# Kernel tuning notes

Measured on AMD Instinct MI355X. Metric: run time of the kernel, lower is better.

Reference implementation:

```python
import jax, jax.numpy as jnp
import numpy as np

N_HEAD = 16
NEG = -1e9


def setup_inputs() -> dict:
    key = jax.random.key(0)
    ks = jax.random.split(key, 10)
    b, s, f = 4, 1024, 1024
    h = N_HEAD
    scale = 1.0 / np.sqrt(f).astype(np.float32)
    x = jax.random.normal(ks[0], (b, s, f), jnp.float32)
    str_mat = jax.random.normal(ks[1], (b, h, s, s), jnp.float32)
    # causal binary mask, float as in the torch module (attn_mask == 0.0 test)
    attn_mask = jnp.broadcast_to(jnp.tril(jnp.ones((s, s), jnp.float32))[None, None], (b, 1, s, s))
    Wq = jax.random.normal(ks[2], (f, f), jnp.float32) * scale
    Wk = jax.random.normal(ks[3], (f, f), jnp.float32) * scale
    Wv = jax.random.normal(ks[4], (f, f), jnp.float32) * scale
    Wo = jax.random.normal(ks[5], (f, f), jnp.float32) * scale
    bq = jax.random.normal(ks[6], (f,), jnp.float32) * 0.01
    bk = jax.random.normal(ks[7], (f,), jnp.float32) * 0.01
    bv = jax.random.normal(ks[8], (f,), jnp.float32) * 0.01
    bo = jax.random.normal(ks[9], (f,), jnp.float32) * 0.01
    return {"x": x, "str_mat": str_mat, "attn_mask": attn_mask,
            "Wq": Wq, "bq": bq, "Wk": Wk, "bk": bk,
            "Wv": Wv, "bv": bv, "Wo": Wo, "bo": bo}


def reference(x, str_mat, attn_mask, Wq, bq, Wk, bk, Wv, bv, Wo, bo):
    b, s, f = x.shape
    h = N_HEAD
    d_h = f // h
    # NOTE: original uses .view(b, h, -1, d_h) with NO transpose -> raw reshape
    q = (x @ Wq + bq).reshape(b, h, s, d_h)
    k = (x @ Wk + bk).reshape(b, h, s, d_h)
    v = (x @ Wv + bv).reshape(b, h, s, d_h)
    # structural bias: mask then softmax
    sm = jnp.where(attn_mask == 0.0, NEG, str_mat)
    sm = jax.nn.softmax(sm, axis=-1)
    # scale by d_h (NOT sqrt(d_h)) as in source; second masked_fill in source
    # is non-in-place with result discarded -> no-op, intentionally omitted
    scores = jnp.einsum('bhqd,bhkd->bhqk', q, k) / d_h + sm
    prob = jax.nn.softmax(scores, axis=-1)  # dropout p=0.0
    out = jnp.einsum('bhqk,bhkd->bhqd', prob, v)  # [b,h,s,d_h]
    out = out.transpose(0, 2, 1, 3).reshape(b, s, f)
    return out @ Wo + bo
```

## Files before the change

### kernel.cpp

```cpp
#include <hip/hip_runtime.h>
#include <hip/hip_bf16.h>

#define BB 4
#define SS 1024
#define FF 1024
#define HH 16
#define DH 64

typedef short bf16x8 __attribute__((ext_vector_type(8)));
typedef float f32x4 __attribute__((ext_vector_type(4)));

__device__ __forceinline__ float b2f(unsigned short u) {
    union { unsigned int i; float f; } x; x.i = ((unsigned int)u) << 16; return x.f;
}
__device__ __forceinline__ unsigned short f2b(float f) {
    unsigned int x = __float_as_uint(f);
    unsigned int r = (x + 0x7fffu + ((x >> 16) & 1u)) >> 16;
    return (unsigned short)r;
}
__device__ __forceinline__ int sw(int row, int col) { return col ^ ((row & 7) << 3); }

__device__ __forceinline__ void async_copy16(void* lds, const void* g) {
    __builtin_amdgcn_global_load_lds(
        (const __attribute__((address_space(1))) unsigned int*)g,
        (__attribute__((address_space(3))) unsigned int*)lds, 16, 0, 0);
}

__global__ void cvt_k(const float* __restrict__ in, unsigned short* __restrict__ out, int n) {
    int i = (blockIdx.x * blockDim.x + threadIdx.x) * 4;
    if (i < n) {
        float4 v = *(const float4*)(in + i);
        ushort4 o;
        o.x = f2b(v.x); o.y = f2b(v.y); o.z = f2b(v.z); o.w = f2b(v.w);
        *(ushort4*)(out + i) = o;
    }
}

__global__ void cvtT_k(const float* __restrict__ W0, const float* __restrict__ W1,
                       const float* __restrict__ W2, const float* __restrict__ W3,
                       unsigned short* __restrict__ out) {
    int y = blockIdx.y;
    const float* src = (y == 0) ? W0 : (y == 1) ? W1 : (y == 2) ? W2 : W3;
    unsigned short* dst = out + (size_t)y * FF * FF;
    __shared__ float t[32][33];
    int tile = blockIdx.x;
    int tk = (tile & 31) * 32, tn = (tile >> 5) * 32;
    int r = threadIdx.x >> 3, c4 = (threadIdx.x & 7) * 4;
    float4 v = *(const float4*)&src[(size_t)(tk + r) * FF + tn + c4];
    t[r][c4 + 0] = v.x; t[r][c4 + 1] = v.y; t[r][c4 + 2] = v.z; t[r][c4 + 3] = v.w;
    __syncthreads();
    ushort4 o;
    o.x = f2b(t[c4 + 0][r]); o.y = f2b(t[c4 + 1][r]);
    o.z = f2b(t[c4 + 2][r]); o.w = f2b(t[c4 + 3][r]);
    *(ushort4*)&dst[(size_t)(tn + r) * FF + tk + c4] = o;
}

__global__ void vtrans_k(const unsigned short* __restrict__ V, unsigned short* __restrict__ Vt) {
    int bh = blockIdx.y;
    int sb = blockIdx.x * 64;
    size_t slab = (size_t)bh * SS * DH;
    __shared__ unsigned int tI[64][65];
    int tid = threadIdx.x;
    #pragma unroll
    for (int v = 0; v < 2; v++) {
        int c = tid + v * 256;
        int row = c >> 3, col = (c & 7) * 8;
        uint4 u = *(const uint4*)&V[slab + (size_t)(sb + row) * DH + col];
        const unsigned short* us = (const unsigned short*)&u;
        #pragma unroll
        for (int j = 0; j < 8; j++) tI[row][col + j] = us[j];
    }
    __syncthreads();
    #pragma unroll
    for (int v = 0; v < 2; v++) {
        int c = tid + v * 256;
        int drow = c >> 3, scol = (c & 7) * 8;
        unsigned short o[8];
        #pragma unroll
        for (int j = 0; j < 8; j++) o[j] = (unsigned short)tI[scol + j][drow];
        *(uint4*)&Vt[slab + (size_t)drow * SS + sb + scol] = *(uint4*)o;
    }
}

__global__ __launch_bounds__(256, 3) void gemm32_k(
    const unsigned short* __restrict__ A, const unsigned short* __restrict__ Wt,
    const float* __restrict__ b0, const float* __restrict__ b1, const float* __restrict__ b2,
    unsigned short* __restrict__ o16)
{
    __shared__ __attribute__((aligned(16))) unsigned short lA[2][128 * 32];
    __shared__ __attribute__((aligned(16))) unsigned short lB[2][128 * 32];

    int tid = threadIdx.x;
    int wave = tid >> 6, lane = tid & 63, quad = lane >> 4, l16 = lane & 15;
    int wm = (wave & 1) * 64, wn = (wave >> 1) * 64;
    int srow = tid >> 2;
    int scol = (tid & 3) * 8;
    int scolsw = scol ^ ((srow & 3) << 3);
    int wv = wave;

    int gy = gridDim.y;
    int bid = blockIdx.y * gridDim.x + blockIdx.x;
    int chunk = (gridDim.x * gy) >> 3;
    int wgid = (bid & 7) * chunk + (bid >> 3);
    int mi_ = wgid / gy, nc = wgid - mi_ * gy;
    int mbase = mi_ * 128;

    int widx = nc >> 3;
    int nbase = (nc & 7) * 128;
    const unsigned short* W = Wt + (size_t)widx * FF * FF;
    const float* bias = (widx == 0) ? b0 : (widx == 1) ? b1 : b2;
    float scale = (widx == 0) ? 0.015625f : 1.0f;
    unsigned short* oq = o16 + (size_t)widx * BB * SS * FF;

    f32x4 acc[4][4];
    #pragma unroll
    for (int i = 0; i < 4; i++)
        #pragma unroll
        for (int j = 0; j < 4; j++) acc[i][j] = (f32x4){0.f, 0.f, 0.f, 0.f};

    const unsigned short* gA = A + (size_t)(mbase + srow) * FF + scolsw;
    const unsigned short* gB = W + (size_t)(nbase + srow) * FF + scolsw;

    #pragma unroll
    for (int i = 0; i < 2; i++) {
        async_copy16((void*)&lA[0][(i * 64 + wv * 16) * 32], gA + (size_t)i * 64 * FF);
        async_copy16((void*)&lB[0][(i * 64 + wv * 16) * 32], gB + (size_t)i * 64 * FF);
    }
    __syncthreads();

    for (int kt = 0; kt < 32; kt++) {
        int cur = kt & 1;
        if (kt < 31) {
            int kb = (kt + 1) * 32;
            #pragma unroll
            for (int i = 0; i < 2; i++) {
                async_copy16((void*)&lA[cur ^ 1][(i * 64 + wv * 16) * 32], gA + (size_t)i * 64 * FF + kb);
                async_copy16((void*)&lB[cur ^ 1][(i * 64 + wv * 16) * 32], gB + (size_t)i * 64 * FF + kb);
            }
        }
        bf16x8 af[4], bfr[4];
        #pragma unroll
        for (int mi = 0; mi < 4; mi++) {
            int row = wm + mi * 16 + l16;
            af[mi] = *(const bf16x8*)(&lA[cur][row * 32 + (quad * 8 ^ ((row & 3) << 3))]);
        }
        #pragma unroll
        for (int ni = 0; ni < 4; ni++) {
            int row = wn + ni * 16 + l16;
            bfr[ni] = *(const bf16x8*)(&lB[cur][row * 32 + (quad * 8 ^ ((row & 3) << 3))]);
        }
        #pragma unroll
        for (int mi = 0; mi < 4; mi++)
            #pragma unroll
            for (int ni = 0; ni < 4; ni++)
                acc[mi][ni] = __builtin_amdgcn_mfma_f32_16x16x32_bf16(af[mi], bfr[ni], acc[mi][ni], 0, 0, 0);
        __syncthreads();
    }

    #pragma unroll
    for (int mi = 0; mi < 4; mi++) {
        #pragma unroll
        for (int ni = 0; ni < 4; ni++) {
            int col = nbase + wn + ni * 16 + l16;
            float bv = bias[col];
            #pragma unroll
            for (int r = 0; r < 4; r++) {
                int row = mbase + wm + mi * 16 + quad * 4 + r;
                float v = (acc[mi][ni][r] + bv) * scale;
                int b_ = row >> 10, i = row & 1023;
                int h = i >> 6, s_ = ((i & 63) << 4) + (col >> 6), d = col & 63;
                oq[(((size_t)(b_ * HH + h)) * SS + s_) * DH + d] = f2b(v);
            }
        }
    }
}

__global__ __launch_bounds__(256, 2) void gemm_k(
    const unsigned short* __restrict__ A, const unsigned short* __restrict__ Wt,
    const float* __restrict__ bias, float* __restrict__ o32)
{
    __shared__ __attribute__((aligned(16))) unsigned short lA[2][128 * 64];
    __shared__ __attribute__((aligned(16))) unsigned short lB[2][128 * 64];

    int tid = threadIdx.x;
    int wave = tid >> 6, lane = tid & 63, quad = lane >> 4, l16 = lane & 15;
    int wm = (wave & 1) * 64, wn = (wave >> 1) * 64;
    int srow = tid >> 3, scol = (tid & 7) * 8;
    int scolsw = scol ^ ((srow & 7) << 3);
    int wv = wave;

    int gy = gridDim.y;
    int bid = blockIdx.y * gridDim.x + blockIdx.x;
    int chunk = (gridDim.x * gy) >> 3;
    int wgid = (bid & 7) * chunk + (bid >> 3);
    int mi_ = wgid / gy, nc = wgid - mi_ * gy;
    int mbase = mi_ * 128;
    int nbase = nc * 128;

    f32x4 acc[4][4];
    #pragma unroll
    for (int i = 0; i < 4; i++)
        #pragma unroll
        for (int j = 0; j < 4; j++) acc[i][j] = (f32x4){0.f, 0.f, 0.f, 0.f};

    const unsigned short* gA = A  + (size_t)(mbase + srow) * FF + scolsw;
    const unsigned short* gB = Wt + (size_t)(nbase + srow) * FF + scolsw;

    #pragma unroll
    for (int i = 0; i < 4; i++) {
        async_copy16((void*)&lA[0][(i * 32 + wv * 8) * 64], gA + (size_t)i * 32 * FF);
        async_copy16((void*)&lB[0][(i * 32 + wv * 8) * 64], gB + (size_t)i * 32 * FF);
    }
    __syncthreads();

    for (int kt = 0; kt < 16; kt++) {
        int cur = kt & 1;
        if (kt < 15) {
            int kb = (kt + 1) * 64;
            #pragma unroll
            for (int i = 0; i < 4; i++) {
                async_copy16((void*)&lA[cur ^ 1][(i * 32 + wv * 8) * 64], gA + (size_t)i * 32 * FF + kb);
                async_copy16((void*)&lB[cur ^ 1][(i * 32 + wv * 8) * 64], gB + (size_t)i * 32 * FF + kb);
            }
        }
        #pragma unroll
        for (int ks = 0; ks < 2; ks++) {
            bf16x8 af[4], bfr[4];
            #pragma unroll
            for (int mi = 0; mi < 4; mi++) {
                int row = wm + mi * 16 + l16;
                af[mi] = *(const bf16x8*)(&lA[cur][row * 64 + sw(row, ks * 32 + quad * 8)]);
            }
            #pragma unroll
            for (int ni = 0; ni < 4; ni++) {
                int row = wn + ni * 16 + l16;
                bfr[ni] = *(const bf16x8*)(&lB[cur][row * 64 + sw(row, ks * 32 + quad * 8)]);
            }
            #pragma unroll
            for (int mi = 0; mi < 4; mi++)
                #pragma unroll
                for (int ni = 0; ni < 4; ni++)
                    acc[mi][ni] = __builtin_amdgcn_mfma_f32_16x16x32_bf16(af[mi], bfr[ni], acc[mi][ni], 0, 0, 0);
        }
        __syncthreads();
    }

    #pragma unroll
    for (int mi = 0; mi < 4; mi++) {
        #pragma unroll
        for (int ni = 0; ni < 4; ni++) {
            int col = nbase + wn + ni * 16 + l16;
            float bv = bias[col];
            #pragma unroll
            for (int r = 0; r < 4; r++) {
                int row = mbase + wm + mi * 16 + quad * 4 + r;
                o32[(size_t)row * FF + col] = acc[mi][ni][r] + bv;
            }
        }
    }
}

__global__ void sm_k(const float* __restrict__ str, unsigned short* __restrict__ smq) {
    int row = blockIdx.x * 4 + (threadIdx.x >> 6);
    int lane = threadIdx.x & 63;
    int r = row & (SS - 1);
    int imax = r >> 8;
    const float* p = str + (size_t)row * SS;
    float vals[16];
    float mx = -1e30f;
    #pragma unroll
    for (int i = 0; i < 4; i++) {
        int k0 = i * 256 + lane * 4;
        if (i <= imax) {
            float4 u = *(const float4*)(&p[k0]);
            float uv[4] = {u.x, u.y, u.z, u.w};
            #pragma unroll
            for (int j = 0; j < 4; j++) {
                float v = (k0 + j <= r) ? uv[j] : -1e30f;
                vals[i * 4 + j] = v;
                mx = fmaxf(mx, v);
            }
        } else {
            #pragma unroll
            for (int j = 0; j < 4; j++) vals[i * 4 + j] = -1e30f;
        }
    }
    #pragma unroll
    for (int d = 1; d < 64; d <<= 1) mx = fmaxf(mx, __shfl_xor(mx, d));
    float sum = 0.f;
    #pragma unroll
    for (int t = 0; t < 16; t++) {
        float e = __expf(fminf(vals[t] - mx, 0.f));
        vals[t] = e;
        sum += e;
    }
    #pragma unroll
    for (int d = 1; d < 64; d <<= 1) sum += __shfl_xor(sum, d);
    float rinv = 1.0f / sum;
    unsigned short* q = smq + (size_t)row * SS;
    #pragma unroll
    for (int i = 0; i < 4; i++) {
        if (i <= imax) {
            ushort4 o;
            o.x = f2b(vals[i * 4 + 0] * rinv);
            o.y = f2b(vals[i * 4 + 1] * rinv);
            o.z = f2b(vals[i * 4 + 2] * rinv);
            o.w = f2b(vals[i * 4 + 3] * rinv);
            *(ushort4*)(&q[i * 256 + lane * 4]) = o;
        }
    }
}

__global__ __launch_bounds__(256, 4) void attn_k(
    const unsigned short* __restrict__ Q, const unsigned short* __restrict__ K,
    const unsigned short* __restrict__ Vt, const unsigned short* __restrict__ sm,
    unsigned short* __restrict__ ctx)
{
    int tid = threadIdx.x;
    int wave = tid >> 6, lane = tid & 63, quad = lane >> 4, l16 = lane & 15;
    int srow = tid >> 3, scol = (tid & 7) * 8;
    int scolsw = scol ^ ((srow & 7) << 3);
    int wv = wave;

    int bid = blockIdx.y * gridDim.x + blockIdx.x;
    int wgid = (bid & 7) * 128 + (bid >> 3);
    int qb = wgid & 15, bh = wgid >> 4;
    int b_ = bh >> 4, h = bh & 15;
    int qbase = qb * 64;

    __shared__ __attribute__((aligned(16))) unsigned short lQP[64 * 64];
    __shared__ __attribute__((aligned(16))) unsigned short lK[2][64 * 64];
    __shared__ __attribute__((aligned(16))) unsigned short lV[2][64 * 64];

    const size_t slab = (size_t)bh * SS * DH;

    #pragma unroll
    for (int v = 0; v < 2; v++) {
        int row = srow + v * 32;
        *(uint4*)&lQP[row * 64 + sw(row, scol)] = *(const uint4*)&Q[slab + (size_t)(qbase + row) * DH + scol];
        async_copy16((void*)&lK[0][(v * 32 + wv * 8) * 64], &K [slab + (size_t)row * DH + scolsw]);
        async_copy16((void*)&lV[0][(v * 32 + wv * 8) * 64], &Vt[slab + (size_t)row * SS + scolsw]);
    }
    int q_loc0 = wave * 16 + quad * 4;
    const size_t smbase = (size_t)bh * SS * SS;
    __syncthreads();

    bf16x8 aq[2];
    #pragma unroll
    for (int ks = 0; ks < 2; ks++) {
        int row = wave * 16 + l16;
        aq[ks] = *(const bf16x8*)&lQP[row * 64 + sw(row, ks * 32 + quad * 8)];
    }

    float l_st[4];
    f32x4 Oacc[4];
    #pragma unroll
    for (int r = 0; r < 4; r++) l_st[r] = 0.f;
    #pragma unroll
    for (int ni = 0; ni < 4; ni++) Oacc[ni] = (f32x4){0.f, 0.f, 0.f, 0.f};

    unsigned short* lPw = &lQP[(wave * 16) * 64];

    for (int tt = 0; tt < 16; tt++) {
        int cur = tt & 1;
        int tbase = tt * 64;
        bool need_sm = (tbase <= qbase);

        if (tt < 15) {
            int nb = tbase + 64;
            #pragma unroll
            for (int v = 0; v < 2; v++) {
                int row = srow + v * 32;
                async_copy16((void*)&lK[cur ^ 1][(v * 32 + wv * 8) * 64], &K [slab + (size_t)(nb + row) * DH + scolsw]);
                async_copy16((void*)&lV[cur ^ 1][(v * 32 + wv * 8) * 64], &Vt[slab + (size_t)row * SS + nb + scolsw]);
            }
        }
        float sf[4][4];
        if (need_sm) {
            #pragma unroll
            for (int r = 0; r < 4; r++) {
                int q_abs = qbase + q_loc0 + r;
                const unsigned short* pr = sm + smbase + (size_t)q_abs * SS + tbase + l16;
                #pragma unroll
                for (int ni = 0; ni < 4; ni++)
                    sf[ni][r] = b2f(pr[ni * 16]);
            }
        }

        f32x4 sa[4];
        #pragma unroll
        for (int ni = 0; ni < 4; ni++) sa[ni] = (f32x4){0.f, 0.f, 0.f, 0.f};
        #pragma unroll
        for (int ks = 0; ks < 2; ks++) {
            #pragma unroll
            for (int ni = 0; ni < 4; ni++) {
                int row = ni * 16 + l16;
                bf16x8 bk_ = *(const bf16x8*)&lK[cur][row * 64 + sw(row, ks * 32 + quad * 8)];
                sa[ni] = __builtin_amdgcn_mfma_f32_16x16x32_bf16(aq[ks], bk_, sa[ni], 0, 0, 0);
            }
        }

        #pragma unroll
        for (int ni = 0; ni < 4; ni++) {
            #pragma unroll
            for (int r = 0; r < 4; r++) {
                float v = sa[ni][r];
                if (need_sm) v += sf[ni][r];
                v = __expf(v);
                sa[ni][r] = v;
                l_st[r] += v;
            }
        }

        #pragma unroll
        for (int ni = 0; ni < 4; ni++) {
            #pragma unroll
            for (int r = 0; r < 4; r += 2) {
                unsigned int pk;
                asm("v_cvt_pk_bf16_f32 %0, %1, %2" : "=v"(pk) : "v"(sa[ni][r]), "v"(sa[ni][r + 1]));
                int r0 = quad * 4 + r;
                int r1 = r0 + 1;
                lPw[r0 * 64 + sw(r0, ni * 16 + l16)] = (unsigned short)pk;
                lPw[r1 * 64 + sw(r1, ni * 16 + l16)] = (unsigned short)(pk >> 16);
            }
        }

        #pragma unroll
        for (int ks = 0; ks < 2; ks++) {
            bf16x8 pa = *(const bf16x8*)&lPw[l16 * 64 + sw(l16, ks * 32 + quad * 8)];
            #pragma unroll
            for (int ni = 0; ni < 4; ni++) {
                int row = ni * 16 + l16;
                bf16x8 bv = *(const bf16x8*)&lV[cur][row * 64 + sw(row, ks * 32 + quad * 8)];
                Oacc[ni] = __builtin_amdgcn_mfma_f32_16x16x32_bf16(pa, bv, Oacc[ni], 0, 0, 0);
            }
        }

        __syncthreads();
    }

    #pragma unroll
    for (int r = 0; r < 4; r++) {
        float v = l_st[r];
        v += __shfl_xor(v, 1); v += __shfl_xor(v, 2);
        v += __shfl_xor(v, 4); v += __shfl_xor(v, 8);
        l_st[r] = v;
    }

    #pragma unroll
    for (int r = 0; r < 4; r++) {
        int s_abs = qbase + wave * 16 + quad * 4 + r;
        float li = 1.0f / l_st[r];
        #pragma unroll
        for (int ni = 0; ni < 4; ni++) {
            int d = ni * 16 + l16;
            ctx[((size_t)b_ * SS + s_abs) * FF + h * 64 + d] = f2b(Oacc[ni][r] * li);
        }
    }
}

extern "C" void kernel_launch(void* const* d_in, const int* in_sizes, int n_in,
                              void* d_out, int out_size, void* d_ws, size_t ws_size,
                              hipStream_t stream) {
    const float* x   = (const float*)d_in[0];
    const float* str = (const float*)d_in[1];
    const float* Wq  = (const float*)d_in[3];
    const float* bq  = (const float*)d_in[4];
    const float* Wk  = (const float*)d_in[5];
    const float* bk  = (const float*)d_in[6];
    const float* Wv  = (const float*)d_in[7];
    const float* bv  = (const float*)d_in[8];
    const float* Wo  = (const float*)d_in[9];
    const float* bo  = (const float*)d_in[10];

    char* ws = (char*)d_ws;
    const size_t MB = 1024ull * 1024;
    unsigned short* xb  = (unsigned short*)ws;
    unsigned short* Wb  = (unsigned short*)(ws + 8 * MB);
    unsigned short* QKV = (unsigned short*)(ws + 16 * MB);
    unsigned short* Vtp = (unsigned short*)(ws + 40 * MB);
    unsigned short* ctx = (unsigned short*)(ws + 48 * MB);
    unsigned short* smb = (unsigned short*)(ws + 64 * MB);

    const size_t QN = (size_t)BB * SS * FF;
    const size_t WN = (size_t)FF * FF;

    cvt_k<<<4096, 256, 0, stream>>>(x, xb, (int)QN);
    cvtT_k<<<dim3(1024, 4), 256, 0, stream>>>(Wq, Wk, Wv, Wo, Wb);

    gemm32_k<<<dim3(32, 24), 256, 0, stream>>>(xb, Wb, bq, bk, bv, QKV);
    vtrans_k<<<dim3(16, 64), 256, 0, stream>>>(QKV + 2 * QN, Vtp);
    sm_k<<<16384, 256, 0, stream>>>(str, smb);
    attn_k<<<dim3(16, 64), 256, 0, stream>>>(QKV, QKV + QN, Vtp, smb, ctx);
    gemm_k<<<dim3(32, 8), 256, 0, stream>>>(ctx, Wb + 3 * WN, bo, (float*)d_out);
}
```

Before: 506.1 us.

## Load K and V tiles directly from global memory instead of LDS staging

```diff
diff --git a/kernel.cpp b/kernel.cpp
--- a/kernel.cpp
+++ b/kernel.cpp
@@ -318,9 +318,6 @@
 {
     int tid = threadIdx.x;
     int wave = tid >> 6, lane = tid & 63, quad = lane >> 4, l16 = lane & 15;
-    int srow = tid >> 3, scol = (tid & 7) * 8;
-    int scolsw = scol ^ ((srow & 7) << 3);
-    int wv = wave;
 
     int bid = blockIdx.y * gridDim.x + blockIdx.x;
     int wgid = (bid & 7) * 128 + (bid >> 3);
@@ -328,29 +325,16 @@
     int b_ = bh >> 4, h = bh & 15;
     int qbase = qb * 64;
 
-    __shared__ __attribute__((aligned(16))) unsigned short lQP[64 * 64];
-    __shared__ __attribute__((aligned(16))) unsigned short lK[2][64 * 64];
-    __shared__ __attribute__((aligned(16))) unsigned short lV[2][64 * 64];
+    __shared__ __attribute__((aligned(16))) unsigned short lP[4][16 * 64];
 
     const size_t slab = (size_t)bh * SS * DH;
-
-    #pragma unroll
-    for (int v = 0; v < 2; v++) {
-        int row = srow + v * 32;
-        *(uint4*)&lQP[row * 64 + sw(row, scol)] = *(const uint4*)&Q[slab + (size_t)(qbase + row) * DH + scol];
-        async_copy16((void*)&lK[0][(v * 32 + wv * 8) * 64], &K [slab + (size_t)row * DH + scolsw]);
-        async_copy16((void*)&lV[0][(v * 32 + wv * 8) * 64], &Vt[slab + (size_t)row * SS + scolsw]);
-    }
+    const size_t smbase = (size_t)bh * SS * SS;
     int q_loc0 = wave * 16 + quad * 4;
-    const size_t smbase = (size_t)bh * SS * SS;
-    __syncthreads();
 
     bf16x8 aq[2];
     #pragma unroll
-    for (int ks = 0; ks < 2; ks++) {
-        int row = wave * 16 + l16;
-        aq[ks] = *(const bf16x8*)&lQP[row * 64 + sw(row, ks * 32 + quad * 8)];
-    }
+    for (int ks = 0; ks < 2; ks++)
+        aq[ks] = *(const bf16x8*)&Q[slab + (size_t)(qbase + wave * 16 + l16) * DH + ks * 32 + quad * 8];
 
     float l_st[4];
     f32x4 Oacc[4];
@@ -359,22 +343,12 @@
     #pragma unroll
     for (int ni = 0; ni < 4; ni++) Oacc[ni] = (f32x4){0.f, 0.f, 0.f, 0.f};
 
-    unsigned short* lPw = &lQP[(wave * 16) * 64];
+    unsigned short* lPw = lP[wave];
 
     for (int tt = 0; tt < 16; tt++) {
-        int cur = tt & 1;
         int tbase = tt * 64;
         bool need_sm = (tbase <= qbase);
 
-        if (tt < 15) {
-            int nb = tbase + 64;
-            #pragma unroll
-            for (int v = 0; v < 2; v++) {
-                int row = srow + v * 32;
-                async_copy16((void*)&lK[cur ^ 1][(v * 32 + wv * 8) * 64], &K [slab + (size_t)(nb + row) * DH + scolsw]);
-                async_copy16((void*)&lV[cur ^ 1][(v * 32 + wv * 8) * 64], &Vt[slab + (size_t)row * SS + nb + scolsw]);
-            }
-        }
         float sf[4][4];
         if (need_sm) {
             #pragma unroll
@@ -394,8 +368,7 @@
         for (int ks = 0; ks < 2; ks++) {
             #pragma unroll
             for (int ni = 0; ni < 4; ni++) {
-                int row = ni * 16 + l16;
-                bf16x8 bk_ = *(const bf16x8*)&lK[cur][row * 64 + sw(row, ks * 32 + quad * 8)];
+                bf16x8 bk_ = *(const bf16x8*)&K[slab + (size_t)(tbase + ni * 16 + l16) * DH + ks * 32 + quad * 8];
                 sa[ni] = __builtin_amdgcn_mfma_f32_16x16x32_bf16(aq[ks], bk_, sa[ni], 0, 0, 0);
             }
         }
@@ -430,13 +403,10 @@
             bf16x8 pa = *(const bf16x8*)&lPw[l16 * 64 + sw(l16, ks * 32 + quad * 8)];
             #pragma unroll
             for (int ni = 0; ni < 4; ni++) {
-                int row = ni * 16 + l16;
-                bf16x8 bv = *(const bf16x8*)&lV[cur][row * 64 + sw(row, ks * 32 + quad * 8)];
+                bf16x8 bv = *(const bf16x8*)&Vt[slab + (size_t)(ni * 16 + l16) * SS + tbase + ks * 32 + quad * 8];
                 Oacc[ni] = __builtin_amdgcn_mfma_f32_16x16x32_bf16(pa, bv, Oacc[ni], 0, 0, 0);
             }
         }
-
-        __syncthreads();
     }
 
     #pragma unroll
```

Measured after the change: 585.1 us. 1.16x slower.
